# Kernel tuning notes

Measured on AMD Instinct MI355X. Metric: run time of the kernel, lower is better.

Reference implementation:

```python
import jax, jax.numpy as jnp
import numpy as np

N, D = 8192, 256
EPS = 1e-12  # guards sqrt(0) on the diagonal


def setup_inputs() -> dict:
    key = jax.random.key(0)
    kx, = jax.random.split(key, 1)
    x = jax.random.normal(kx, (N, D), dtype=jnp.float32)
    threshold = jnp.zeros((1,), dtype=jnp.float32)  # nn.Parameter(torch.zeros(1))
    t = jnp.ones((1,), dtype=jnp.float32)           # nn.Parameter(torch.ones(1))
    return {"x": x, "threshold": threshold, "t": t}


def reference(x, threshold, t):
    # Sigmoid-like branch: pairwise euclidean distance without materializing [N,N,D].
    # |x_i - x_j|^2 summed over D == ||x_i||^2 + ||x_j||^2 - 2 x_i.x_j  (abs is a no-op under squaring)
    sq = jnp.sum(x * x, axis=1)  # [N]
    dist2 = sq[:, None] + sq[None, :] - 2.0 * (x @ x.T)  # [N, N]
    dist = jnp.sqrt(jnp.maximum(dist2, EPS))
    diff = (dist + threshold) * t  # broadcast scalar params
    return 1.0 - jax.nn.sigmoid(diff)
```

## Files before the change

### kernel.cpp

```cpp
#include <hip/hip_runtime.h>
#include <cstdint>
#include <cstddef>

#define NN 8192
#define DD 256

typedef __bf16 bf16x8 __attribute__((ext_vector_type(8)));
typedef float f32x16 __attribute__((ext_vector_type(16)));
typedef unsigned short ushort8 __attribute__((ext_vector_type(8)));

__global__ __launch_bounds__(256) void prep_kernel(const float* __restrict__ x,
                                                   unsigned short* __restrict__ xbt,
                                                   float* __restrict__ sq) {
    const int t = threadIdx.x;
    const int oct = t & 31;
    const int rl = t >> 5;
    const int row = blockIdx.x * 8 + rl;
    const float4* xp = (const float4*)(x + (size_t)row * DD + oct * 8);
    const float4 a = xp[0], b = xp[1];
    const float vs[8] = {a.x, a.y, a.z, a.w, b.x, b.y, b.z, b.w};
    ushort8 o;
    float p = 0.0f;
#pragma unroll
    for (int i = 0; i < 8; ++i) {
        const float v = vs[i];
        const unsigned int u = __float_as_uint(v);
        o[i] = (unsigned short)((u + 0x7FFFu + ((u >> 16) & 1u)) >> 16);
        p = fmaf(v, v, p);
    }
    *(ushort8*)(xbt + ((size_t)oct * NN + row) * 8) = o;
#pragma unroll
    for (int off = 16; off > 0; off >>= 1) p += __shfl_down(p, off, 32);
    if (oct == 0) sq[row] = p;
}

__global__ __launch_bounds__(256, 4) void gemm_sig_kernel(
    const unsigned short* __restrict__ XbT, const float* __restrict__ sq,
    const float* __restrict__ thrp, const float* __restrict__ tp,
    float* __restrict__ out) {
    const int tid = threadIdx.x;
    const int wave = tid >> 6;
    const int lane = tid & 63;
    const int m = lane & 31;
    const int q2 = lane >> 5;

    const int brow = blockIdx.y;
    const int bcol = blockIdx.x;
    const int wrow = (wave >> 1) * 64;
    const int wcol = (wave & 1) * 64;

    const uint32_t rowA0 = (uint32_t)brow * 128;
    const uint32_t rowB0 = (uint32_t)bcol * 128;

    const uint32_t offA = ((uint32_t)q2 * NN + rowA0 + wrow + m) * 8;
    const uint32_t offB = ((uint32_t)q2 * NN + rowB0 + wcol + m) * 8;
    const uint32_t kkS = 2u * NN * 8;

    f32x16 acc[2][2] = {};
    bf16x8 af[2][2], bfv[2][2];

#pragma unroll
    for (int t = 0; t < 2; ++t) {
        af[0][t]  = *(const bf16x8*)(XbT + offA + t * 256);
        bfv[0][t] = *(const bf16x8*)(XbT + offB + t * 256);
    }
#pragma unroll
    for (int kk = 0; kk < 16; ++kk) {
        const int cur = kk & 1, nxt = cur ^ 1;
        if (kk < 15) {
            const uint32_t ko = (uint32_t)(kk + 1) * kkS;
#pragma unroll
            for (int t = 0; t < 2; ++t) {
                af[nxt][t]  = *(const bf16x8*)(XbT + offA + ko + t * 256);
                bfv[nxt][t] = *(const bf16x8*)(XbT + offB + ko + t * 256);
            }
        }
#pragma unroll
        for (int ti = 0; ti < 2; ++ti)
#pragma unroll
            for (int tj = 0; tj < 2; ++tj)
                acc[ti][tj] = __builtin_amdgcn_mfma_f32_32x32x16_bf16(
                    af[cur][ti], bfv[cur][tj], acc[ti][tj], 0, 0, 0);
    }

    const float tv = tp[0];
    const float thr_t = thrp[0] * tv;
    const uint32_t colg0 = rowB0 + wcol + m;

#pragma unroll
    for (int ti = 0; ti < 2; ++ti) {
        const uint32_t rbase = rowA0 + wrow + ti * 32 + 4 * q2;
        float sqi[16];
#pragma unroll
        for (int rg = 0; rg < 16; ++rg)
            sqi[rg] = sq[rbase + (rg & 3) + 8 * (rg >> 2)];
#pragma unroll
        for (int tj = 0; tj < 2; ++tj) {
            const uint32_t colg = colg0 + tj * 32;
            const float sqj = sq[colg];
#pragma unroll
            for (int rg = 0; rg < 16; ++rg) {
                const uint32_t r = rbase + (rg & 3) + 8 * (rg >> 2);
                float d2 = fmaf(-2.0f, acc[ti][tj][rg], sqi[rg] + sqj);
                if (r == colg) d2 = 0.0f;
                d2 = fmaxf(d2, 1e-12f);
                const float dist = __builtin_amdgcn_sqrtf(d2);
                const float e = __expf(fmaf(dist, tv, thr_t));
                out[(size_t)r * NN + colg] = __builtin_amdgcn_rcpf(1.0f + e);
            }
        }
    }
}

extern "C" void kernel_launch(void* const* d_in, const int* in_sizes, int n_in,
                              void* d_out, int out_size, void* d_ws, size_t ws_size,
                              hipStream_t stream) {
    const float* x = (const float*)d_in[0];
    const float* threshold = (const float*)d_in[1];
    const float* t = (const float*)d_in[2];
    float* out = (float*)d_out;

    unsigned short* xbt = (unsigned short*)d_ws;
    float* sq = (float*)((char*)d_ws + (size_t)NN * DD * sizeof(unsigned short));

    prep_kernel<<<NN / 8, 256, 0, stream>>>(x, xbt, sq);
    dim3 grid(NN / 128, NN / 128);
    gemm_sig_kernel<<<grid, 256, 0, stream>>>(xbt, sq, threshold, t, out);
}
```

Before: 286.8 us.

## Shrink per-wave tile to 32x64 and block tile to 128x64 for occupancy

Each wave now computes a 32x64 output tile (two MFMAs per k-step) instead of 64x64, and the block covers 128 rows by 64 columns, so the grid doubles along x. Accumulator and fragment registers are halved, and the launch bound is raised to 5 waves-per-EU hint so more waves can be resident to hide global-load latency and the store-heavy epilogue. The cost is lower register-level reuse of the B fragments across rows, giving more global loads per MFMA.

```diff
diff --git a/kernel.cpp b/kernel.cpp
--- a/kernel.cpp
+++ b/kernel.cpp
@@ -34,7 +34,7 @@
     if (oct == 0) sq[row] = p;
 }
 
-__global__ __launch_bounds__(256, 4) void gemm_sig_kernel(
+__global__ __launch_bounds__(256, 5) void gemm_sig_kernel(
     const unsigned short* __restrict__ XbT, const float* __restrict__ sq,
     const float* __restrict__ thrp, const float* __restrict__ tp,
     float* __restrict__ out) {
@@ -44,70 +44,55 @@
     const int m = lane & 31;
     const int q2 = lane >> 5;
 
-    const int brow = blockIdx.y;
-    const int bcol = blockIdx.x;
-    const int wrow = (wave >> 1) * 64;
-    const int wcol = (wave & 1) * 64;
+    const uint32_t rowA0 = (uint32_t)blockIdx.y * 128 + (uint32_t)wave * 32;
+    const uint32_t colB0 = (uint32_t)blockIdx.x * 64;
 
-    const uint32_t rowA0 = (uint32_t)brow * 128;
-    const uint32_t rowB0 = (uint32_t)bcol * 128;
-
-    const uint32_t offA = ((uint32_t)q2 * NN + rowA0 + wrow + m) * 8;
-    const uint32_t offB = ((uint32_t)q2 * NN + rowB0 + wcol + m) * 8;
+    const uint32_t offA = ((uint32_t)q2 * NN + rowA0 + m) * 8;
+    const uint32_t offB = ((uint32_t)q2 * NN + colB0 + m) * 8;
     const uint32_t kkS = 2u * NN * 8;
 
-    f32x16 acc[2][2] = {};
-    bf16x8 af[2][2], bfv[2][2];
+    f32x16 acc[2] = {};
+    bf16x8 af[2], bf[2][2];
 
-#pragma unroll
-    for (int t = 0; t < 2; ++t) {
-        af[0][t]  = *(const bf16x8*)(XbT + offA + t * 256);
-        bfv[0][t] = *(const bf16x8*)(XbT + offB + t * 256);
-    }
+    af[0]    = *(const bf16x8*)(XbT + offA);
+    bf[0][0] = *(const bf16x8*)(XbT + offB);
+    bf[0][1] = *(const bf16x8*)(XbT + offB + 256);
+
 #pragma unroll
     for (int kk = 0; kk < 16; ++kk) {
         const int cur = kk & 1, nxt = cur ^ 1;
         if (kk < 15) {
             const uint32_t ko = (uint32_t)(kk + 1) * kkS;
-#pragma unroll
-            for (int t = 0; t < 2; ++t) {
-                af[nxt][t]  = *(const bf16x8*)(XbT + offA + ko + t * 256);
-                bfv[nxt][t] = *(const bf16x8*)(XbT + offB + ko + t * 256);
-            }
+            af[nxt]    = *(const bf16x8*)(XbT + offA + ko);
+            bf[nxt][0] = *(const bf16x8*)(XbT + offB + ko);
+            bf[nxt][1] = *(const bf16x8*)(XbT + offB + ko + 256);
         }
-#pragma unroll
-        for (int ti = 0; ti < 2; ++ti)
-#pragma unroll
-            for (int tj = 0; tj < 2; ++tj)
-                acc[ti][tj] = __builtin_amdgcn_mfma_f32_32x32x16_bf16(
-                    af[cur][ti], bfv[cur][tj], acc[ti][tj], 0, 0, 0);
+        acc[0] = __builtin_amdgcn_mfma_f32_32x32x16_bf16(af[cur], bf[cur][0], acc[0], 0, 0, 0);
+        acc[1] = __builtin_amdgcn_mfma_f32_32x32x16_bf16(af[cur], bf[cur][1], acc[1], 0, 0, 0);
     }
 
     const float tv = tp[0];
     const float thr_t = thrp[0] * tv;
-    const uint32_t colg0 = rowB0 + wcol + m;
+
+    const uint32_t rbase = rowA0 + 4 * q2;
+    float sqi[16];
+#pragma unroll
+    for (int rg = 0; rg < 16; ++rg)
+        sqi[rg] = sq[rbase + (rg & 3) + 8 * (rg >> 2)];
 
 #pragma unroll
-    for (int ti = 0; ti < 2; ++ti) {
-        const uint32_t rbase = rowA0 + wrow + ti * 32 + 4 * q2;
-        float sqi[16];
+    for (int tj = 0; tj < 2; ++tj) {
+        const uint32_t colg = colB0 + tj * 32 + m;
+        const float sqj = sq[colg];
 #pragma unroll
-        for (int rg = 0; rg < 16; ++rg)
-            sqi[rg] = sq[rbase + (rg & 3) + 8 * (rg >> 2)];
-#pragma unroll
-        for (int tj = 0; tj < 2; ++tj) {
-            const uint32_t colg = colg0 + tj * 32;
-            const float sqj = sq[colg];
-#pragma unroll
-            for (int rg = 0; rg < 16; ++rg) {
-                const uint32_t r = rbase + (rg & 3) + 8 * (rg >> 2);
-                float d2 = fmaf(-2.0f, acc[ti][tj][rg], sqi[rg] + sqj);
-                if (r == colg) d2 = 0.0f;
-                d2 = fmaxf(d2, 1e-12f);
-                const float dist = __builtin_amdgcn_sqrtf(d2);
-                const float e = __expf(fmaf(dist, tv, thr_t));
-                out[(size_t)r * NN + colg] = __builtin_amdgcn_rcpf(1.0f + e);
-            }
+        for (int rg = 0; rg < 16; ++rg) {
+            const uint32_t r = rbase + (rg & 3) + 8 * (rg >> 2);
+            float d2 = fmaf(-2.0f, acc[tj][rg], sqi[rg] + sqj);
+            if (r == colg) d2 = 0.0f;
+            d2 = fmaxf(d2, 1e-12f);
+            const float dist = __builtin_amdgcn_sqrtf(d2);
+            const float e = __expf(fmaf(dist, tv, thr_t));
+            out[(size_t)r * NN + colg] = __builtin_amdgcn_rcpf(1.0f + e);
         }
     }
 }
@@ -124,6 +109,6 @@
     float* sq = (float*)((char*)d_ws + (size_t)NN * DD * sizeof(unsigned short));
 
     prep_kernel<<<NN / 8, 256, 0, stream>>>(x, xbt, sq);
-    dim3 grid(NN / 128, NN / 128);
+    dim3 grid(NN / 64, NN / 128);
     gemm_sig_kernel<<<grid, 256, 0, stream>>>(xbt, sq, threshold, t, out);
 }
```

New measurement: 298.2 us. 4.0% more time.
